# Kernel tuning notes

Measured on AMD Instinct MI355X. Metric: run time of the kernel, lower is better.

The kernel has to match this reference:

```python
import jax, jax.numpy as jnp
import numpy as np

N = 50000
F_DIM = 128
H_DIM = 128
E = 800000


def setup_inputs() -> dict:
    key = jax.random.key(0)
    ks = jax.random.split(key, 8)
    x = jax.random.normal(ks[0], (N, F_DIM), dtype=jnp.float32)
    edge_weight = jax.random.uniform(ks[1], (E,), dtype=jnp.float32)
    src = jax.random.randint(ks[2], (E,), 0, N)
    dst = jax.random.randint(ks[3], (E,), 0, N)
    edge_index = jnp.stack([src, dst]).astype(jnp.int64)
    sc = 1.0 / np.sqrt(F_DIM)
    W1 = jax.random.normal(ks[4], (F_DIM, H_DIM), dtype=jnp.float32) * sc
    W2 = jax.random.normal(ks[5], (H_DIM, H_DIM), dtype=jnp.float32) * sc
    Wfc = jax.random.normal(ks[6], (H_DIM, F_DIM), dtype=jnp.float32) * sc
    b1 = jnp.zeros((H_DIM,), jnp.float32)
    b2 = jnp.zeros((H_DIM,), jnp.float32)
    bfc = jnp.zeros((F_DIM,), jnp.float32)
    return {"x": x, "edge_weight": edge_weight, "W1": W1, "b1": b1,
            "W2": W2, "b2": b2, "Wfc": Wfc, "bfc": bfc,
            "edge_index": edge_index}


def _gcn_norm(src, dst, edge_weight, num_nodes):
    # PyG gcn_norm: add self-loops (weight 1), symmetric D^-1/2 A D^-1/2
    loop = jnp.arange(num_nodes, dtype=src.dtype)
    src2 = jnp.concatenate([src, loop])
    dst2 = jnp.concatenate([dst, loop])
    w2 = jnp.concatenate([edge_weight, jnp.ones((num_nodes,), edge_weight.dtype)])
    deg = jax.ops.segment_sum(w2, dst2, num_segments=num_nodes)
    dinv = jnp.where(deg > 0, jax.lax.rsqrt(jnp.where(deg > 0, deg, 1.0)), 0.0)
    norm = dinv[src2] * w2 * dinv[dst2]
    return src2, dst2, norm


def _gcn_conv(x, W, b, src, dst, norm, num_nodes):
    h = x @ W                              # [N, out]
    msg = norm[:, None] * h[src]           # gather + scale, [E+N, out]
    agg = jax.ops.segment_sum(msg, dst, num_segments=num_nodes)
    return agg + b


def reference(x, edge_weight, W1, b1, W2, b2, Wfc, bfc, edge_index):
    src, dst = edge_index[0], edge_index[1]
    src2, dst2, norm = _gcn_norm(src, dst, edge_weight, N)
    h = jax.nn.relu(_gcn_conv(x, W1, b1, src2, dst2, norm, N))
    h = jax.nn.relu(_gcn_conv(h, W2, b2, src2, dst2, norm, N))
    return h @ Wfc + bfc
```

## Files before the change

kernel.cpp:

```cpp
#include <hip/hip_runtime.h>
#include <hip/hip_fp16.h>


typedef unsigned long long u64;
typedef _Float16 f16x8 __attribute__((ext_vector_type(8)));
typedef float f32x4 __attribute__((ext_vector_type(4)));

#define CAP 96

__global__ __launch_bounds__(256) void k_pre(unsigned* cnt, int n,
                                             const float* __restrict__ W1,
                                             const float* __restrict__ W2,
                                             const float* __restrict__ Wfc,
                                             __half* __restrict__ Wt) {
    int i = blockIdx.x * 256 + threadIdx.x;
    if (i < n) cnt[i] = 0u;
    if (i < 3 * 16384) {
        int w = i >> 14, r = i & 16383;
        int nn = r >> 7, kk = r & 127;
        const float* W = (w == 0) ? W1 : (w == 1) ? W2 : Wfc;
        Wt[i] = __float2half(W[kk * 128 + nn]);
    }
}

__global__ __launch_bounds__(256) void k_bucket(const int* __restrict__ src,
                                                const int* __restrict__ dst,
                                                const float* __restrict__ ew,
                                                unsigned* __restrict__ cnt,
                                                int2* __restrict__ slots, int E) {
    int e = blockIdx.x * 256 + threadIdx.x;
    if (e < E) {
        int d = dst[e];
        unsigned pos = atomicAdd(&cnt[d], 1u);
        if (pos < CAP)
            slots[(size_t)d * CAP + pos] = make_int2(src[e], __float_as_int(ew[e]));
    }
}

__global__ __launch_bounds__(256) void k_deg(const int2* __restrict__ slots,
                                             const unsigned* __restrict__ cnt,
                                             float* __restrict__ dinv, int n) {
    int wid = (blockIdx.x * 256 + threadIdx.x) >> 6;
    int lane = threadIdx.x & 63;
    if (wid >= n) return;
    int i = __builtin_amdgcn_readfirstlane(wid);
    int c = min((int)cnt[i], CAP);
    float w = 0.f;
    if (lane < c) w = __int_as_float(slots[(size_t)i * CAP + lane].y);
#pragma unroll
    for (int off = 32; off > 0; off >>= 1) w += __shfl_xor(w, off);
    if (lane == 0) dinv[i] = rsqrtf(1.0f + w);
}

template <bool IN_FP32, bool OUT_HALF>
__global__ __launch_bounds__(256) void k_gemm(const void* __restrict__ Xv,
                                              const __half* __restrict__ Wt,
                                              const float* __restrict__ bias,
                                              void* __restrict__ Yv, int n) {
    __shared__ __align__(16) _Float16 Ws[128][136];
    int t = threadIdx.x;
    for (int i = t; i < 2048; i += 256) {
        int r = i >> 4, c8 = (i & 15) << 3;
        *(f16x8*)&Ws[r][c8] = *(const f16x8*)((const _Float16*)Wt + r * 128 + c8);
    }
    __syncthreads();

    int wave = t >> 6, lane = t & 63;
    int quad = lane >> 4, fcol = lane & 15;
    int rowbase = blockIdx.x * 64 + wave * 16;
    int arow = rowbase + fcol;

    f16x8 a[4];
#pragma unroll
    for (int c = 0; c < 4; c++) {
        int k0 = c * 32 + quad * 8;
        if (arow < n) {
            if (IN_FP32) {
                const float* p = (const float*)Xv + (size_t)arow * 128 + k0;
#pragma unroll
                for (int j = 0; j < 8; j++) a[c][j] = (_Float16)p[j];
            } else {
                a[c] = *(const f16x8*)((const _Float16*)Xv + (size_t)arow * 128 + k0);
            }
        } else {
            f16x8 z = {0, 0, 0, 0, 0, 0, 0, 0};
            a[c] = z;
        }
    }

    f32x4 acc[8];
#pragma unroll
    for (int c = 0; c < 8; c++) acc[c] = (f32x4){0.f, 0.f, 0.f, 0.f};

#pragma unroll
    for (int kc = 0; kc < 4; kc++) {
        int k0 = kc * 32 + quad * 8;
#pragma unroll
        for (int ct = 0; ct < 8; ct++) {
            f16x8 b = *(const f16x8*)&Ws[ct * 16 + fcol][k0];
            acc[ct] = __builtin_amdgcn_mfma_f32_16x16x32_f16(a[kc], b, acc[ct], 0, 0, 0);
        }
    }

#pragma unroll
    for (int reg = 0; reg < 4; reg++) {
        int gr = rowbase + quad * 4 + reg;
        if (gr < n) {
            if (OUT_HALF) {
                __half* Y = (__half*)Yv;
#pragma unroll
                for (int ct = 0; ct < 8; ct++)
                    Y[(size_t)gr * 128 + ct * 16 + fcol] = __float2half(acc[ct][reg]);
            } else {
                float* Y = (float*)Yv;
#pragma unroll
                for (int ct = 0; ct < 8; ct++)
                    Y[(size_t)gr * 128 + ct * 16 + fcol] = acc[ct][reg] + bias[ct * 16 + fcol];
            }
        }
    }
}

__global__ __launch_bounds__(256) void k_agg(const __half* __restrict__ H,
                                             const int2* __restrict__ slots,
                                             const unsigned* __restrict__ cnt,
                                             const float* __restrict__ dinv,
                                             const float* __restrict__ bias,
                                             __half* __restrict__ out, int n) {
    int wid = (blockIdx.x * 256 + threadIdx.x) >> 6;
    int lane = threadIdx.x & 63;
    if (wid >= n) return;
    int i = __builtin_amdgcn_readfirstlane(wid);
    float di = dinv[i];
    float2 h0 = __half22float2(((const __half2*)(H + (size_t)i * 128))[lane]);
    float ax = di * di * h0.x, ay = di * di * h0.y;
    int c = min((int)cnt[i], CAP);
    const int2* row = slots + (size_t)i * CAP;

    for (int base = 0; base < c; base += 64) {
        int cnt2 = min(64, c - base);
        int mys = 0; float myv = 0.f;
        if (lane < cnt2) {
            int2 pr = row[base + lane];
            mys = pr.x;
            myv = dinv[pr.x] * __int_as_float(pr.y) * di;
        }
        int j = 0;
        for (; j + 16 <= cnt2; j += 16) {
            float2 h[16];
            float v[16];
#pragma unroll
            for (int u = 0; u < 16; u++) {
                int s = __shfl(mys, j + u);
                v[u] = __shfl(myv, j + u);
                h[u] = __half22float2(((const __half2*)(H + (size_t)s * 128))[lane]);
            }
#pragma unroll
            for (int u = 0; u < 16; u++) {
                ax = fmaf(v[u], h[u].x, ax);
                ay = fmaf(v[u], h[u].y, ay);
            }
        }
        for (; j < cnt2; j += 8) {
            float2 h[8];
            float v[8];
#pragma unroll
            for (int u = 0; u < 8; u++) {
                int idx = j + u;
                int lsrc = min(idx, cnt2 - 1);
                int s = __shfl(mys, lsrc);
                float tv = __shfl(myv, lsrc);
                v[u] = (idx < cnt2) ? tv : 0.f;
                h[u] = __half22float2(((const __half2*)(H + (size_t)s * 128))[lane]);
            }
#pragma unroll
            for (int u = 0; u < 8; u++) {
                ax = fmaf(v[u], h[u].x, ax);
                ay = fmaf(v[u], h[u].y, ay);
            }
        }
    }
    float2 b = ((const float2*)bias)[lane];
    ax = fmaxf(ax + b.x, 0.f);
    ay = fmaxf(ay + b.y, 0.f);
    ((__half2*)(out + (size_t)i * 128))[lane] = __floats2half2_rn(ax, ay);
}

extern "C" void kernel_launch(void* const* d_in, const int* in_sizes, int n_in,
                              void* d_out, int out_size, void* d_ws, size_t ws_size,
                              hipStream_t stream) {
    const float* x   = (const float*)d_in[0];
    const float* ew  = (const float*)d_in[1];
    const float* W1  = (const float*)d_in[2];
    const float* b1  = (const float*)d_in[3];
    const float* W2  = (const float*)d_in[4];
    const float* b2  = (const float*)d_in[5];
    const float* Wfc = (const float*)d_in[6];
    const float* bfc = (const float*)d_in[7];
    const int* eidx  = (const int*)d_in[8];

    const int E = in_sizes[1];
    const int N = in_sizes[0] / 128;
    const int* src = eidx;
    const int* dst = eidx + E;

    char* ws = (char*)d_ws;
    size_t off = 0;
    auto alloc = [&](size_t bytes) -> void* {
        void* p = ws + off;
        off = (off + bytes + 255) & ~(size_t)255;
        return p;
    };
    int eb = (E + 255) / 256;
    int gb = (N + 63) / 64;
    int ab = (N * 64 + 255) / 256;
    int pb = (max(N, 3 * 16384) + 255) / 256;
    int Npad = N + 64;

    unsigned* cnt  = (unsigned*)alloc((size_t)N * 4);
    float*  dinv   = (float*)alloc((size_t)N * 4);
    int2*   slots  = (int2*)alloc((size_t)N * CAP * 8);
    __half* Wt     = (__half*)alloc((size_t)3 * 16384 * 2);
    __half* bufH   = (__half*)alloc((size_t)Npad * 128 * 2);
    __half* bufA   = (__half*)alloc((size_t)Npad * 128 * 2);

    k_pre<<<pb, 256, 0, stream>>>(cnt, N, W1, W2, Wfc, Wt);
    k_bucket<<<eb, 256, 0, stream>>>(src, dst, ew, cnt, slots, E);
    k_deg<<<ab, 256, 0, stream>>>(slots, cnt, dinv, N);

    k_gemm<true, true><<<gb, 256, 0, stream>>>(x, Wt, nullptr, bufH, N);
    k_agg<<<ab, 256, 0, stream>>>(bufH, slots, cnt, dinv, b1, bufA, N);
    k_gemm<false, true><<<gb, 256, 0, stream>>>(bufA, Wt + 16384, nullptr, bufH, N);
    k_agg<<<ab, 256, 0, stream>>>(bufH, slots, cnt, dinv, b2, bufA, N);
    k_gemm<false, false><<<gb, 256, 0, stream>>>(bufA, Wt + 2 * 16384, bfc, d_out, N);
}
```

Baseline: 242.4 us.

## Fuse first GEMM with edge bucketing into one launch and batch bucket atomics

The edge-bucketing kernel and the first-layer GEMM are merged into one launch. Low block indices run the GEMM and higher ones bucket edges, so the bandwidth-bound atomic scatter overlaps with the MFMA GEMM and one launch disappears. Each bucketing thread now handles four edges, issuing all loads and atomics before the stores to raise memory-level parallelism. The bucket blocks allocate the GEMM's shared-memory tile even though they never use it, which may reduce occupancy.

```diff
diff --git a/kernel.cpp b/kernel.cpp
--- a/kernel.cpp
+++ b/kernel.cpp
@@ -23,18 +23,116 @@
     }
 }
 
-__global__ __launch_bounds__(256) void k_bucket(const int* __restrict__ src,
-                                                const int* __restrict__ dst,
-                                                const float* __restrict__ ew,
-                                                unsigned* __restrict__ cnt,
-                                                int2* __restrict__ slots, int E) {
-    int e = blockIdx.x * 256 + threadIdx.x;
-    if (e < E) {
-        int d = dst[e];
-        unsigned pos = atomicAdd(&cnt[d], 1u);
-        if (pos < CAP)
-            slots[(size_t)d * CAP + pos] = make_int2(src[e], __float_as_int(ew[e]));
-    }
+template <bool IN_FP32, bool OUT_HALF>
+__device__ __forceinline__ void gemm_body(int bx, const void* __restrict__ Xv,
+                                          const __half* __restrict__ Wt,
+                                          const float* __restrict__ bias,
+                                          void* __restrict__ Yv, int n) {
+    __shared__ __align__(16) _Float16 Ws[128][136];
+    int t = threadIdx.x;
+    for (int i = t; i < 2048; i += 256) {
+        int r = i >> 4, c8 = (i & 15) << 3;
+        *(f16x8*)&Ws[r][c8] = *(const f16x8*)((const _Float16*)Wt + r * 128 + c8);
+    }
+    __syncthreads();
+
+    int wave = t >> 6, lane = t & 63;
+    int quad = lane >> 4, fcol = lane & 15;
+    int rowbase = bx * 64 + wave * 16;
+    int arow = rowbase + fcol;
+
+    f16x8 a[4];
+#pragma unroll
+    for (int c = 0; c < 4; c++) {
+        int k0 = c * 32 + quad * 8;
+        if (arow < n) {
+            if (IN_FP32) {
+                const float* p = (const float*)Xv + (size_t)arow * 128 + k0;
+#pragma unroll
+                for (int j = 0; j < 8; j++) a[c][j] = (_Float16)p[j];
+            } else {
+                a[c] = *(const f16x8*)((const _Float16*)Xv + (size_t)arow * 128 + k0);
+            }
+        } else {
+            f16x8 z = {0, 0, 0, 0, 0, 0, 0, 0};
+            a[c] = z;
+        }
+    }
+
+    f32x4 acc[8];
+#pragma unroll
+    for (int c = 0; c < 8; c++) acc[c] = (f32x4){0.f, 0.f, 0.f, 0.f};
+
+#pragma unroll
+    for (int kc = 0; kc < 4; kc++) {
+        int k0 = kc * 32 + quad * 8;
+#pragma unroll
+        for (int ct = 0; ct < 8; ct++) {
+            f16x8 b = *(const f16x8*)&Ws[ct * 16 + fcol][k0];
+            acc[ct] = __builtin_amdgcn_mfma_f32_16x16x32_f16(a[kc], b, acc[ct], 0, 0, 0);
+        }
+    }
+
+#pragma unroll
+    for (int reg = 0; reg < 4; reg++) {
+        int gr = rowbase + quad * 4 + reg;
+        if (gr < n) {
+            if (OUT_HALF) {
+                __half* Y = (__half*)Yv;
+#pragma unroll
+                for (int ct = 0; ct < 8; ct++)
+                    Y[(size_t)gr * 128 + ct * 16 + fcol] = __float2half(acc[ct][reg]);
+            } else {
+                float* Y = (float*)Yv;
+#pragma unroll
+                for (int ct = 0; ct < 8; ct++)
+                    Y[(size_t)gr * 128 + ct * 16 + fcol] = acc[ct][reg] + bias[ct * 16 + fcol];
+            }
+        }
+    }
+}
+
+template <bool IN_FP32, bool OUT_HALF>
+__global__ __launch_bounds__(256) void k_gemm(const void* __restrict__ Xv,
+                                              const __half* __restrict__ Wt,
+                                              const float* __restrict__ bias,
+                                              void* __restrict__ Yv, int n) {
+    gemm_body<IN_FP32, OUT_HALF>(blockIdx.x, Xv, Wt, bias, Yv, n);
+}
+
+__global__ __launch_bounds__(256) void k_gemm1_bucket(
+    const float* __restrict__ x, const __half* __restrict__ Wt,
+    __half* __restrict__ bufH, int n, int GB,
+    const int* __restrict__ src, const int* __restrict__ dst,
+    const float* __restrict__ ew, unsigned* __restrict__ cnt,
+    int2* __restrict__ slots, int E) {
+    int bx = blockIdx.x;
+    if (bx < GB) {
+        gemm_body<true, true>(bx, x, Wt, nullptr, bufH, n);
+        return;
+    }
+    int base = (bx - GB) * 1024 + threadIdx.x;
+    int e0 = base, e1 = base + 256, e2 = base + 512, e3 = base + 768;
+    int s4[4], d4[4];
+    float w4[4];
+    int ee[4] = {e0, e1, e2, e3};
+#pragma unroll
+    for (int k = 0; k < 4; k++) {
+        if (ee[k] < E) {
+            s4[k] = src[ee[k]];
+            d4[k] = dst[ee[k]];
+            w4[k] = ew[ee[k]];
+        }
+    }
+    unsigned pos[4];
+#pragma unroll
+    for (int k = 0; k < 4; k++)
+        if (ee[k] < E) pos[k] = atomicAdd(&cnt[d4[k]], 1u);
+#pragma unroll
+    for (int k = 0; k < 4; k++)
+        if (ee[k] < E && pos[k] < CAP)
+            slots[(size_t)d4[k] * CAP + pos[k]] =
+                make_int2(s4[k], __float_as_int(w4[k]));
 }
 
 __global__ __launch_bounds__(256) void k_deg(const int2* __restrict__ slots,
@@ -50,75 +148,6 @@
 #pragma unroll
     for (int off = 32; off > 0; off >>= 1) w += __shfl_xor(w, off);
     if (lane == 0) dinv[i] = rsqrtf(1.0f + w);
-}
-
-template <bool IN_FP32, bool OUT_HALF>
-__global__ __launch_bounds__(256) void k_gemm(const void* __restrict__ Xv,
-                                              const __half* __restrict__ Wt,
-                                              const float* __restrict__ bias,
-                                              void* __restrict__ Yv, int n) {
-    __shared__ __align__(16) _Float16 Ws[128][136];
-    int t = threadIdx.x;
-    for (int i = t; i < 2048; i += 256) {
-        int r = i >> 4, c8 = (i & 15) << 3;
-        *(f16x8*)&Ws[r][c8] = *(const f16x8*)((const _Float16*)Wt + r * 128 + c8);
-    }
-    __syncthreads();
-
-    int wave = t >> 6, lane = t & 63;
-    int quad = lane >> 4, fcol = lane & 15;
-    int rowbase = blockIdx.x * 64 + wave * 16;
-    int arow = rowbase + fcol;
-
-    f16x8 a[4];
-#pragma unroll
-    for (int c = 0; c < 4; c++) {
-        int k0 = c * 32 + quad * 8;
-        if (arow < n) {
-            if (IN_FP32) {
-                const float* p = (const float*)Xv + (size_t)arow * 128 + k0;
-#pragma unroll
-                for (int j = 0; j < 8; j++) a[c][j] = (_Float16)p[j];
-            } else {
-                a[c] = *(const f16x8*)((const _Float16*)Xv + (size_t)arow * 128 + k0);
-            }
-        } else {
-            f16x8 z = {0, 0, 0, 0, 0, 0, 0, 0};
-            a[c] = z;
-        }
-    }
-
-    f32x4 acc[8];
-#pragma unroll
-    for (int c = 0; c < 8; c++) acc[c] = (f32x4){0.f, 0.f, 0.f, 0.f};
-
-#pragma unroll
-    for (int kc = 0; kc < 4; kc++) {
-        int k0 = kc * 32 + quad * 8;
-#pragma unroll
-        for (int ct = 0; ct < 8; ct++) {
-            f16x8 b = *(const f16x8*)&Ws[ct * 16 + fcol][k0];
-            acc[ct] = __builtin_amdgcn_mfma_f32_16x16x32_f16(a[kc], b, acc[ct], 0, 0, 0);
-        }
-    }
-
-#pragma unroll
-    for (int reg = 0; reg < 4; reg++) {
-        int gr = rowbase + quad * 4 + reg;
-        if (gr < n) {
-            if (OUT_HALF) {
-                __half* Y = (__half*)Yv;
-#pragma unroll
-                for (int ct = 0; ct < 8; ct++)
-                    Y[(size_t)gr * 128 + ct * 16 + fcol] = __float2half(acc[ct][reg]);
-            } else {
-                float* Y = (float*)Yv;
-#pragma unroll
-                for (int ct = 0; ct < 8; ct++)
-                    Y[(size_t)gr * 128 + ct * 16 + fcol] = acc[ct][reg] + bias[ct * 16 + fcol];
-            }
-        }
-    }
 }
 
 __global__ __launch_bounds__(256) void k_agg(const __half* __restrict__ H,
@@ -211,8 +240,8 @@
         off = (off + bytes + 255) & ~(size_t)255;
         return p;
     };
-    int eb = (E + 255) / 256;
     int gb = (N + 63) / 64;
+    int eb4 = (E + 1023) / 1024;
     int ab = (N * 64 + 255) / 256;
     int pb = (max(N, 3 * 16384) + 255) / 256;
     int Npad = N + 64;
@@ -225,10 +254,10 @@
     __half* bufA   = (__half*)alloc((size_t)Npad * 128 * 2);
 
     k_pre<<<pb, 256, 0, stream>>>(cnt, N, W1, W2, Wfc, Wt);
-    k_bucket<<<eb, 256, 0, stream>>>(src, dst, ew, cnt, slots, E);
+    k_gemm1_bucket<<<gb + eb4, 256, 0, stream>>>(x, Wt, bufH, N, gb,
+                                                 src, dst, ew, cnt, slots, E);
     k_deg<<<ab, 256, 0, stream>>>(slots, cnt, dinv, N);
 
-    k_gemm<true, true><<<gb, 256, 0, stream>>>(x, Wt, nullptr, bufH, N);
     k_agg<<<ab, 256, 0, stream>>>(bufH, slots, cnt, dinv, b1, bufA, N);
     k_gemm<false, true><<<gb, 256, 0, stream>>>(bufA, Wt + 16384, nullptr, bufH, N);
     k_agg<<<ab, 256, 0, stream>>>(bufH, slots, cnt, dinv, b2, bufA, N);
```

Result: faster. 233.0 us (-3.9%).
